# Kernel optimization log

Hardware: AMD Instinct MI355X
Metric: run time of the kernel (lower is better)

Reference implementation:

```python
import jax, jax.numpy as jnp
import numpy as np

B_SZ, SEQ, D_MODEL = 64, 2048, 12
D_INNER, D_STATE, D_CONV, DT_RANK = 24, 16, 4, 4


def setup_inputs() -> dict:
    key = jax.random.key(0)
    ks = jax.random.split(key, 10)
    def n(k, shape, scale):
        return jax.random.normal(k, shape, jnp.float32) * scale
    return {
        "x": jax.random.normal(ks[0], (B_SZ, SEQ, D_MODEL), jnp.float32),
        "in_proj_w": n(ks[1], (2 * D_INNER, D_MODEL), 0.2),
        "conv_w": n(ks[2], (D_INNER, 1, D_CONV), 0.3),
        "conv_b": jnp.zeros((D_INNER,), jnp.float32),
        "x_proj_w": n(ks[3], (DT_RANK + 2 * D_STATE, D_INNER), 0.2),
        "dt_proj_w": n(ks[4], (D_INNER, DT_RANK), 0.5),
        "dt_proj_b": jax.random.uniform(ks[5], (D_INNER,), jnp.float32, -4.0, -2.0),
        "A_log": jnp.log(jnp.broadcast_to(jnp.arange(1, D_STATE + 1, dtype=jnp.float32), (D_INNER, D_STATE))),
        "D": jnp.ones((D_INNER,), jnp.float32),
        "out_proj_w": n(ks[6], (D_MODEL, D_INNER), 0.2),
        "fc_w": n(ks[7], (1, D_MODEL), 0.3),
        "fc_b": jnp.zeros((1,), jnp.float32),
    }


def _silu(v):
    return v * jax.nn.sigmoid(v)


def _mamba_head(x, in_proj_w, conv_w, conv_b, x_proj_w, dt_proj_w, dt_proj_b,
                A_log, D, out_proj_w, fc_w, fc_b):
    di = A_log.shape[0]
    ds = A_log.shape[1]
    dtr = dt_proj_w.shape[1]
    dc = conv_w.shape[-1]
    bsz = x.shape[0]

    # input projection -> [B,L,2*di], split into ssm branch and gate
    xz = jnp.einsum('bld,ed->ble', x, in_proj_w)
    x_in, z = jnp.split(xz, 2, axis=-1)

    # causal depthwise conv1d over time
    x_t = jnp.transpose(x_in, (0, 2, 1))                       # [B,di,L]
    x_t = jnp.pad(x_t, ((0, 0), (0, 0), (dc - 1, 0)))
    xc = jax.lax.conv_general_dilated(x_t, conv_w, (1,), 'VALID',
                                      feature_group_count=di)
    xc = _silu(jnp.transpose(xc + conv_b[None, :, None], (0, 2, 1)))  # [B,L,di]

    # data-dependent dt, B, C
    x_dbl = jnp.einsum('bld,ed->ble', xc, x_proj_w)
    dt, Bm, Cm = jnp.split(x_dbl, [dtr, dtr + ds], axis=-1)
    dt = jax.nn.softplus(jnp.einsum('blr,dr->bld', dt, dt_proj_w) + dt_proj_b)  # [B,L,di]

    A = -jnp.exp(A_log)                                        # [di,ds]
    dA = jnp.exp(dt[..., None] * A)                            # [B,L,di,ds]
    dBu = dt[..., None] * Bm[:, :, None, :] * xc[..., None]    # [B,L,di,ds]

    def step(h, inp):
        dA_t, dBu_t, C_t = inp
        h = dA_t * h + dBu_t                                   # [B,di,ds]
        y = jnp.einsum('bds,bs->bd', h, C_t)
        return h, y

    h0 = jnp.zeros((bsz, di, ds), x.dtype)
    _, ys = jax.lax.scan(step, h0, (jnp.swapaxes(dA, 0, 1),
                                    jnp.swapaxes(dBu, 0, 1),
                                    jnp.swapaxes(Cm, 0, 1)))
    y = jnp.swapaxes(ys, 0, 1) + xc * D                        # [B,L,di]
    y = y * _silu(z)
    out = jnp.einsum('bld,ed->ble', y, out_proj_w)             # [B,L,d_model]

    # final head on last timestep (SimpleMamba.linear)
    pred = out[:, -1, :] @ fc_w.T + fc_b                       # [B,1]
    return pred


def reference(x, in_proj_w, conv_w, conv_b, x_proj_w, dt_proj_w, dt_proj_b,
              A_log, D, out_proj_w, fc_w, fc_b):
    return _mamba_head(x, in_proj_w, conv_w, conv_b, x_proj_w, dt_proj_w,
                       dt_proj_b, A_log, D, out_proj_w, fc_w, fc_b)
```

## Files before the change

kernel.cpp:

```cpp
#include <hip/hip_runtime.h>
#include <math.h>

#define B_SZ 64
#define SEQ 2048
#define DM 12
#define DI 24
#define DS 16
#define DC 4
#define DTR 4
#define NSEG 32
#define SEGLEN 64
#define LP 68

__device__ __forceinline__ float silu_f(float v) { return v / (1.f + __expf(-v)); }
__device__ __forceinline__ float softplus_f(float v) {
    return fmaxf(v, 0.f) + __logf(1.f + __expf(-fabsf(v)));
}
__device__ __forceinline__ float dot12w(float4 w0, float4 w1, float4 w2,
                                        float4 r0, float4 r1, float4 r2) {
    float s = 0.f;
    s = fmaf(w0.x, r0.x, s); s = fmaf(w0.y, r0.y, s);
    s = fmaf(w0.z, r0.z, s); s = fmaf(w0.w, r0.w, s);
    s = fmaf(w1.x, r1.x, s); s = fmaf(w1.y, r1.y, s);
    s = fmaf(w1.z, r1.z, s); s = fmaf(w1.w, r1.w, s);
    s = fmaf(w2.x, r2.x, s); s = fmaf(w2.y, r2.y, s);
    s = fmaf(w2.z, r2.z, s); s = fmaf(w2.w, r2.w, s);
    return s;
}

__global__ __launch_bounds__(64) void fused_wave_kernel(
    const float* __restrict__ x, const float* __restrict__ ipw,
    const float* __restrict__ cw, const float* __restrict__ cb,
    const float* __restrict__ xpw, const float* __restrict__ dpw,
    const float* __restrict__ dpb, const float* __restrict__ A_log,
    float* __restrict__ segA, float* __restrict__ segB)
{
    __shared__ __align__(16) float dts_s[DI][LP];
    __shared__ __align__(16) float dus_s[DI][LP];
    __shared__ __align__(16) float Bs_s[DS][LP];

    const int lane = threadIdx.x;
    const int b = blockIdx.x >> 5, seg = blockIdx.x & 31;
    const int t0 = seg * SEGLEN;
    const int t = lane;

#pragma unroll
    for (int rep = 0; rep < 2; ++rep) {
        int pp = lane + rep * 64;
        if (pp < 3 * DI) {
            int hr = pp / DI, d = pp % DI;
            int row = t0 - 3 + hr;
            float v = 0.f;
            if (row >= 0) {
                const float4* xp = (const float4*)(x + ((size_t)b * SEQ + row) * DM);
                const float4* wp = (const float4*)(ipw + d * DM);
                v = dot12w(wp[0], wp[1], wp[2], xp[0], xp[1], xp[2]);
            }
            dus_s[d][hr] = v;
        }
    }

    {
        const float4* xp = (const float4*)(x + ((size_t)b * SEQ + (t0 + t)) * DM);
        float4 r0 = xp[0], r1 = xp[1], r2 = xp[2];
#pragma unroll
        for (int d = 0; d < DI; ++d) {
            const float4* wp = (const float4*)(ipw + d * DM);
            dus_s[d][t + 3] = dot12w(wp[0], wp[1], wp[2], r0, r1, r2);
        }
    }
    __syncthreads();

    float xc[DI];
#pragma unroll
    for (int d = 0; d < DI; ++d) {
        const float4 c4 = *(const float4*)(cw + d * DC);
        float acc = cb[d];
        acc = fmaf(c4.x, dus_s[d][t + 0], acc);
        acc = fmaf(c4.y, dus_s[d][t + 1], acc);
        acc = fmaf(c4.z, dus_s[d][t + 2], acc);
        acc = fmaf(c4.w, dus_s[d][t + 3], acc);
        xc[d] = silu_f(acc);
    }
    __syncthreads();

    float dt_raw[DTR];
#pragma unroll
    for (int r = 0; r < DTR + DS; ++r) {
        const float4* wr = (const float4*)(xpw + r * DI);
        float s = 0.f;
#pragma unroll
        for (int c = 0; c < 6; ++c) {
            float4 w4 = wr[c];
            s = fmaf(w4.x, xc[4 * c + 0], s);
            s = fmaf(w4.y, xc[4 * c + 1], s);
            s = fmaf(w4.z, xc[4 * c + 2], s);
            s = fmaf(w4.w, xc[4 * c + 3], s);
        }
        if (r < DTR) dt_raw[r] = s;
        else         Bs_s[r - DTR][t] = s;
    }

#pragma unroll
    for (int d = 0; d < DI; ++d) {
        const float4 w4 = *(const float4*)(dpw + d * DTR);
        float sv = dpb[d];
        sv = fmaf(dt_raw[0], w4.x, sv); sv = fmaf(dt_raw[1], w4.y, sv);
        sv = fmaf(dt_raw[2], w4.z, sv); sv = fmaf(dt_raw[3], w4.w, sv);
        float dt = softplus_f(sv);
        dts_s[d][t] = dt;
        dus_s[d][t] = dt * xc[d];
    }
    __syncthreads();

    {
        const int s_ = lane & 15;
        const int db = lane >> 4;
        float Ap[6], aa[6], ba[6];
#pragma unroll
        for (int p = 0; p < 6; ++p) {
            Ap[p] = -__expf(A_log[(4 * p + db) * DS + s_]);
            aa[p] = 1.f; ba[p] = 0.f;
        }
#pragma unroll 2
        for (int i = 0; i < SEGLEN / 4; ++i) {
            const float4 B4 = *(const float4*)&Bs_s[s_][4 * i];
#pragma unroll
            for (int p = 0; p < 6; ++p) {
                const int d = 4 * p + db;
                const float4 dt4 = *(const float4*)&dts_s[d][4 * i];
                const float4 du4 = *(const float4*)&dus_s[d][4 * i];
                float a;
                a = __expf(dt4.x * Ap[p]); ba[p] = fmaf(a, ba[p], du4.x * B4.x); aa[p] *= a;
                a = __expf(dt4.y * Ap[p]); ba[p] = fmaf(a, ba[p], du4.y * B4.y); aa[p] *= a;
                a = __expf(dt4.z * Ap[p]); ba[p] = fmaf(a, ba[p], du4.z * B4.z); aa[p] *= a;
                a = __expf(dt4.w * Ap[p]); ba[p] = fmaf(a, ba[p], du4.w * B4.w); aa[p] *= a;
            }
        }
        const size_t base = (size_t)blockIdx.x * (DI * DS);
#pragma unroll
        for (int p = 0; p < 6; ++p) {
            segA[base + 64 * p + lane] = aa[p];
            segB[base + 64 * p + lane] = ba[p];
        }
    }
}

__global__ __launch_bounds__(384) void finish_kernel(
    const float* __restrict__ segA, const float* __restrict__ segB,
    const float* __restrict__ x, const float* __restrict__ ipw,
    const float* __restrict__ cw, const float* __restrict__ cb,
    const float* __restrict__ xpw, const float* __restrict__ Dv,
    const float* __restrict__ opw, const float* __restrict__ fcw,
    const float* __restrict__ fcb, float* __restrict__ out)
{
    int b = blockIdx.x, tid = threadIdx.x;

    float h = 0.f;
#pragma unroll
    for (int g = 0; g < NSEG; ++g) {
        size_t o = ((size_t)(b * NSEG + g)) * (DI * DS) + tid;
        h = fmaf(segA[o], h, segB[o]);
    }

    __shared__ float h_sh[DI * DS];
    __shared__ float xcl[DI], CL[DS], zv[DI], yv[DI], ov[DM];
    h_sh[tid] = h;

    const float* xr = x + ((size_t)b * SEQ + SEQ - 1) * DM;
    if (tid < DI) {
        float acc = cb[tid];
#pragma unroll
        for (int k = 0; k < DC; ++k) {
            const float* row = x + ((size_t)b * SEQ + (SEQ - DC + k)) * DM;
            float xin = 0.f;
#pragma unroll
            for (int m = 0; m < DM; ++m) xin = fmaf(row[m], ipw[tid * DM + m], xin);
            acc = fmaf(xin, cw[tid * DC + k], acc);
        }
        xcl[tid] = silu_f(acc);
        float s = 0.f;
#pragma unroll
        for (int m = 0; m < DM; ++m) s = fmaf(xr[m], ipw[(DI + tid) * DM + m], s);
        zv[tid] = s;
    }
    __syncthreads();

    if (tid < DS) {
        float s = 0.f;
#pragma unroll
        for (int d = 0; d < DI; ++d) s = fmaf(xcl[d], xpw[(DTR + DS + tid) * DI + d], s);
        CL[tid] = s;
    }
    __syncthreads();

    if (tid < DI) {
        float y = 0.f;
#pragma unroll
        for (int s2 = 0; s2 < DS; ++s2) y = fmaf(h_sh[tid * DS + s2], CL[s2], y);
        y = fmaf(xcl[tid], Dv[tid], y);
        yv[tid] = y * silu_f(zv[tid]);
    }
    __syncthreads();

    if (tid < DM) {
        float s = 0.f;
#pragma unroll
        for (int d = 0; d < DI; ++d) s = fmaf(yv[d], opw[tid * DI + d], s);
        ov[tid] = s;
    }
    __syncthreads();

    if (tid == 0) {
        float s = fcb[0];
#pragma unroll
        for (int e = 0; e < DM; ++e) s = fmaf(ov[e], fcw[e], s);
        out[b] = s;
    }
}

extern "C" void kernel_launch(void* const* d_in, const int* in_sizes, int n_in,
                              void* d_out, int out_size, void* d_ws, size_t ws_size,
                              hipStream_t stream)
{
    const float* x   = (const float*)d_in[0];
    const float* ipw = (const float*)d_in[1];
    const float* cw  = (const float*)d_in[2];
    const float* cb  = (const float*)d_in[3];
    const float* xpw = (const float*)d_in[4];
    const float* dpw = (const float*)d_in[5];
    const float* dpb = (const float*)d_in[6];
    const float* Al  = (const float*)d_in[7];
    const float* Dv  = (const float*)d_in[8];
    const float* opw = (const float*)d_in[9];
    const float* fcw = (const float*)d_in[10];
    const float* fcb = (const float*)d_in[11];

    float* segA = (float*)d_ws;
    float* segB = segA + (size_t)B_SZ * NSEG * DI * DS;

    fused_wave_kernel<<<B_SZ * NSEG, 64, 0, stream>>>(
        x, ipw, cw, cb, xpw, dpw, dpb, Al, segA, segB);
    finish_kernel<<<B_SZ, 384, 0, stream>>>(
        segA, segB, x, ipw, cw, cb, xpw, Dv, opw, fcw, fcb, (float*)d_out);
}
```

Measured before the change: 109.5 us.

## Split per-segment work across two wavefronts with 128-thread blocks

The fused segment kernel now launches 128 threads per block instead of 64. Each half-wave group handles 12 of the 24 inner channels for the projection, conv and dt stages, and the x_proj rows are split 10/10 between the halves. Intermediates are passed through shared memory, which adds one extra barrier and an LDS round trip for xc and dt_raw. In the scan each thread now carries 3 (d,s) states instead of 6, shortening the serial chain per thread while doubling the thread count per block.

```diff
diff --git a/kernel.cpp b/kernel.cpp
--- a/kernel.cpp
+++ b/kernel.cpp
@@ -28,108 +28,120 @@
     return s;
 }
 
-__global__ __launch_bounds__(64) void fused_wave_kernel(
+__global__ __launch_bounds__(128) void fused2_kernel(
     const float* __restrict__ x, const float* __restrict__ ipw,
     const float* __restrict__ cw, const float* __restrict__ cb,
     const float* __restrict__ xpw, const float* __restrict__ dpw,
     const float* __restrict__ dpb, const float* __restrict__ A_log,
     float* __restrict__ segA, float* __restrict__ segB)
 {
-    __shared__ __align__(16) float dts_s[DI][LP];
-    __shared__ __align__(16) float dus_s[DI][LP];
+    __shared__ __align__(16) float dtxc_s[DI][LP];
+    __shared__ __align__(16) float duxin_s[DI][LP];
     __shared__ __align__(16) float Bs_s[DS][LP];
-
-    const int lane = threadIdx.x;
+    __shared__ __align__(16) float dtr_s[DTR][LP];
+
+    const int tid = threadIdx.x;
     const int b = blockIdx.x >> 5, seg = blockIdx.x & 31;
     const int t0 = seg * SEGLEN;
-    const int t = lane;
-
-#pragma unroll
-    for (int rep = 0; rep < 2; ++rep) {
-        int pp = lane + rep * 64;
-        if (pp < 3 * DI) {
-            int hr = pp / DI, d = pp % DI;
-            int row = t0 - 3 + hr;
-            float v = 0.f;
-            if (row >= 0) {
-                const float4* xp = (const float4*)(x + ((size_t)b * SEQ + row) * DM);
-                const float4* wp = (const float4*)(ipw + d * DM);
-                v = dot12w(wp[0], wp[1], wp[2], xp[0], xp[1], xp[2]);
-            }
-            dus_s[d][hr] = v;
-        }
+    const int t = tid & 63;
+    const int half = tid >> 6;
+    const int dlo = half * 12;
+
+    if (tid < 3 * DI) {
+        int hr = tid / DI, d = tid % DI;
+        int row = t0 - 3 + hr;
+        float v = 0.f;
+        if (row >= 0) {
+            const float4* xp = (const float4*)(x + ((size_t)b * SEQ + row) * DM);
+            const float4* wp = (const float4*)(ipw + d * DM);
+            v = dot12w(wp[0], wp[1], wp[2], xp[0], xp[1], xp[2]);
+        }
+        duxin_s[d][hr] = v;
     }
 
     {
         const float4* xp = (const float4*)(x + ((size_t)b * SEQ + (t0 + t)) * DM);
         float4 r0 = xp[0], r1 = xp[1], r2 = xp[2];
 #pragma unroll
-        for (int d = 0; d < DI; ++d) {
-            const float4* wp = (const float4*)(ipw + d * DM);
-            dus_s[d][t + 3] = dot12w(wp[0], wp[1], wp[2], r0, r1, r2);
-        }
-    }
-    __syncthreads();
-
-    float xc[DI];
-#pragma unroll
-    for (int d = 0; d < DI; ++d) {
+        for (int i = 0; i < 12; ++i) {
+            const float4* wp = (const float4*)(ipw + (dlo + i) * DM);
+            duxin_s[dlo + i][t + 3] = dot12w(wp[0], wp[1], wp[2], r0, r1, r2);
+        }
+    }
+    __syncthreads();
+
+    float xc_reg[12];
+#pragma unroll
+    for (int i = 0; i < 12; ++i) {
+        int d = dlo + i;
         const float4 c4 = *(const float4*)(cw + d * DC);
         float acc = cb[d];
-        acc = fmaf(c4.x, dus_s[d][t + 0], acc);
-        acc = fmaf(c4.y, dus_s[d][t + 1], acc);
-        acc = fmaf(c4.z, dus_s[d][t + 2], acc);
-        acc = fmaf(c4.w, dus_s[d][t + 3], acc);
-        xc[d] = silu_f(acc);
-    }
-    __syncthreads();
-
-    float dt_raw[DTR];
-#pragma unroll
-    for (int r = 0; r < DTR + DS; ++r) {
-        const float4* wr = (const float4*)(xpw + r * DI);
-        float s = 0.f;
-#pragma unroll
-        for (int c = 0; c < 6; ++c) {
-            float4 w4 = wr[c];
-            s = fmaf(w4.x, xc[4 * c + 0], s);
-            s = fmaf(w4.y, xc[4 * c + 1], s);
-            s = fmaf(w4.z, xc[4 * c + 2], s);
-            s = fmaf(w4.w, xc[4 * c + 3], s);
-        }
-        if (r < DTR) dt_raw[r] = s;
-        else         Bs_s[r - DTR][t] = s;
-    }
-
-#pragma unroll
-    for (int d = 0; d < DI; ++d) {
-        const float4 w4 = *(const float4*)(dpw + d * DTR);
-        float sv = dpb[d];
-        sv = fmaf(dt_raw[0], w4.x, sv); sv = fmaf(dt_raw[1], w4.y, sv);
-        sv = fmaf(dt_raw[2], w4.z, sv); sv = fmaf(dt_raw[3], w4.w, sv);
-        float dt = softplus_f(sv);
-        dts_s[d][t] = dt;
-        dus_s[d][t] = dt * xc[d];
-    }
-    __syncthreads();
-
-    {
-        const int s_ = lane & 15;
-        const int db = lane >> 4;
-        float Ap[6], aa[6], ba[6];
-#pragma unroll
-        for (int p = 0; p < 6; ++p) {
-            Ap[p] = -__expf(A_log[(4 * p + db) * DS + s_]);
+        acc = fmaf(c4.x, duxin_s[d][t + 0], acc);
+        acc = fmaf(c4.y, duxin_s[d][t + 1], acc);
+        acc = fmaf(c4.z, duxin_s[d][t + 2], acc);
+        acc = fmaf(c4.w, duxin_s[d][t + 3], acc);
+        float v = silu_f(acc);
+        xc_reg[i] = v;
+        dtxc_s[d][t] = v;
+    }
+    __syncthreads();
+
+    {
+        float xcv[DI];
+#pragma unroll
+        for (int d = 0; d < DI; ++d) xcv[d] = dtxc_s[d][t];
+#pragma unroll
+        for (int q = 0; q < 10; ++q) {
+            int r = half * 10 + q;
+            const float4* wr = (const float4*)(xpw + r * DI);
+            float s = 0.f;
+#pragma unroll
+            for (int c = 0; c < 6; ++c) {
+                float4 w4 = wr[c];
+                s = fmaf(w4.x, xcv[4 * c + 0], s);
+                s = fmaf(w4.y, xcv[4 * c + 1], s);
+                s = fmaf(w4.z, xcv[4 * c + 2], s);
+                s = fmaf(w4.w, xcv[4 * c + 3], s);
+            }
+            if (r < DTR) dtr_s[r][t] = s;
+            else         Bs_s[r - DTR][t] = s;
+        }
+    }
+    __syncthreads();
+
+    {
+        float d0 = dtr_s[0][t], d1 = dtr_s[1][t], d2 = dtr_s[2][t], d3 = dtr_s[3][t];
+#pragma unroll
+        for (int i = 0; i < 12; ++i) {
+            int d = dlo + i;
+            const float4 w4 = *(const float4*)(dpw + d * DTR);
+            float sv = dpb[d];
+            sv = fmaf(d0, w4.x, sv); sv = fmaf(d1, w4.y, sv);
+            sv = fmaf(d2, w4.z, sv); sv = fmaf(d3, w4.w, sv);
+            float dt = softplus_f(sv);
+            dtxc_s[d][t] = dt;
+            duxin_s[d][t] = dt * xc_reg[i];
+        }
+    }
+    __syncthreads();
+
+    {
+        const int s_ = tid & 15;
+        const int dq = tid >> 4;
+        float Ap[3], aa[3], ba[3];
+#pragma unroll
+        for (int p = 0; p < 3; ++p) {
+            Ap[p] = -__expf(A_log[128 * p + tid]);
             aa[p] = 1.f; ba[p] = 0.f;
         }
-#pragma unroll 2
+#pragma unroll 4
         for (int i = 0; i < SEGLEN / 4; ++i) {
             const float4 B4 = *(const float4*)&Bs_s[s_][4 * i];
 #pragma unroll
-            for (int p = 0; p < 6; ++p) {
-                const int d = 4 * p + db;
-                const float4 dt4 = *(const float4*)&dts_s[d][4 * i];
-                const float4 du4 = *(const float4*)&dus_s[d][4 * i];
+            for (int p = 0; p < 3; ++p) {
+                const int d = 8 * p + dq;
+                const float4 dt4 = *(const float4*)&dtxc_s[d][4 * i];
+                const float4 du4 = *(const float4*)&duxin_s[d][4 * i];
                 float a;
                 a = __expf(dt4.x * Ap[p]); ba[p] = fmaf(a, ba[p], du4.x * B4.x); aa[p] *= a;
                 a = __expf(dt4.y * Ap[p]); ba[p] = fmaf(a, ba[p], du4.y * B4.y); aa[p] *= a;
@@ -139,9 +151,9 @@
         }
         const size_t base = (size_t)blockIdx.x * (DI * DS);
 #pragma unroll
-        for (int p = 0; p < 6; ++p) {
-            segA[base + 64 * p + lane] = aa[p];
-            segB[base + 64 * p + lane] = ba[p];
+        for (int p = 0; p < 3; ++p) {
+            segA[base + 128 * p + tid] = aa[p];
+            segB[base + 128 * p + tid] = ba[p];
         }
     }
 }
@@ -239,7 +251,7 @@
     float* segA = (float*)d_ws;
     float* segB = segA + (size_t)B_SZ * NSEG * DI * DS;
 
-    fused_wave_kernel<<<B_SZ * NSEG, 64, 0, stream>>>(
+    fused2_kernel<<<B_SZ * NSEG, 128, 0, stream>>>(
         x, ipw, cw, cb, xpw, dpw, dpb, Al, segA, segB);
     finish_kernel<<<B_SZ, 384, 0, stream>>>(
         segA, segB, x, ipw, cw, cb, xpw, Dv, opw, fcw, fcb, (float*)d_out);
```

After: 106.8 us. -2.5%, faster.
